# Kernel tuning notes

Hardware: AMD Instinct MI355X
Metric: run time of the kernel (lower is better)

Reference implementation:

```python
import jax, jax.numpy as jnp
import numpy as np

D_MODEL = 2048
D_LATENT = 512


def setup_inputs() -> dict:
    key = jax.random.key(0)
    ks = jax.random.split(key, 6)
    x = jax.random.normal(ks[0], (2, 4096, D_MODEL), dtype=jnp.float32)
    cache = jax.random.normal(ks[1], (2, 4096, D_LATENT), dtype=jnp.float32)
    s = 0.02
    # weights stored (in_features, out_features); equivalent to torch Linear (no bias)
    W_kv = jax.random.normal(ks[2], (D_MODEL, D_LATENT), dtype=jnp.float32) * s
    W_q = jax.random.normal(ks[3], (D_MODEL, D_MODEL), dtype=jnp.float32) * s
    W_lq = jax.random.normal(ks[4], (D_MODEL, D_LATENT), dtype=jnp.float32) * s
    W_o = jax.random.normal(ks[5], (D_LATENT, D_MODEL), dtype=jnp.float32) * s
    return {"x": x, "cache": cache, "W_kv": W_kv, "W_q": W_q, "W_lq": W_lq, "W_o": W_o}


def reference(x, cache, W_kv, W_q, W_lq, W_o):
    # latent compression of inputs: (B, S, d_latent)
    l_kv_new = jnp.einsum('bsd,dl->bsl', x, W_kv)
    # query path: x -> query (d_model) -> latent query (d_latent)
    q = jnp.einsum('bsd,de->bse', x, W_q)
    lq = jnp.einsum('bse,el->bsl', q, W_lq)
    # append to cache: (B, T+S, d_latent)
    l_kv = jnp.concatenate([cache, l_kv_new], axis=1)
    scale = jnp.sqrt(jnp.float32(D_LATENT)).astype(x.dtype)
    # attention in latent space: scores (B, S, T+S)
    scores = jnp.einsum('bsl,btl->bst', lq, l_kv) / scale
    weights = jax.nn.softmax(scores, axis=-1)
    ctx = jnp.einsum('bst,btl->bsl', weights, l_kv)
    out = jnp.einsum('bsl,ld->bsd', ctx, W_o)
    return out, l_kv
```

## Files before the change

kernel.cpp:

```cpp
#include <hip/hip_runtime.h>
#include <hip/hip_bf16.h>
#include <math.h>


typedef _Float16 f16x8 __attribute__((ext_vector_type(8)));
typedef _Float16 f16x4 __attribute__((ext_vector_type(4)));
typedef float    f32x4 __attribute__((ext_vector_type(4)));
typedef float    f32x8 __attribute__((ext_vector_type(8)));

__device__ __forceinline__ void gl_lds16(const void* g, void* l) {
  __builtin_amdgcn_global_load_lds(
      (const __attribute__((address_space(1))) void*)g,
      (__attribute__((address_space(3))) void*)l, 16, 0, 0);
}

__global__ __launch_bounds__(256) void k_cache(const float* __restrict__ cache,
                                               float* __restrict__ lkv_f32,
                                               _Float16* __restrict__ lkv16, int n4) {
  int i = blockIdx.x * blockDim.x + threadIdx.x;
  int st = gridDim.x * blockDim.x;
  for (; i < n4; i += st) {
    f32x4 v = reinterpret_cast<const f32x4*>(cache)[i];
    int e = i << 2;
    int b = e >> 21;
    int dst = e + (b << 21);
    *reinterpret_cast<f32x4*>(lkv_f32 + dst) = v;
    *reinterpret_cast<f16x4*>(lkv16 + dst) = __builtin_convertvector(v, f16x4);
  }
}

__global__ __launch_bounds__(256) void k_tc(const float* __restrict__ in,
                                            _Float16* __restrict__ out, int R, int C) {
  __shared__ float t[32][33];
  const int c0 = blockIdx.x << 5, r0 = blockIdx.y << 5;
  const int tid = threadIdx.x;
  {
    int r = tid >> 3, c4 = (tid & 7) << 2;
    f32x4 v = *reinterpret_cast<const f32x4*>(&in[(long)(r0 + r) * C + c0 + c4]);
    t[r][c4] = v[0]; t[r][c4 + 1] = v[1]; t[r][c4 + 2] = v[2]; t[r][c4 + 3] = v[3];
  }
  __syncthreads();
  {
    int c = tid >> 3, r4 = (tid & 7) << 2;
    f16x4 o = {(_Float16)t[r4][c], (_Float16)t[r4 + 1][c],
               (_Float16)t[r4 + 2][c], (_Float16)t[r4 + 3][c]};
    *reinterpret_cast<f16x4*>(&out[(long)(c0 + c) * R + r0 + r4]) = o;
  }
}

__global__ __launch_bounds__(256) void k_tb(const _Float16* __restrict__ in,
                                            _Float16* __restrict__ out, int R, int C) {
  __shared__ _Float16 t[32][36];
  const int c0 = blockIdx.x << 5, r0 = blockIdx.y << 5;
  const int tid = threadIdx.x;
  {
    int r = tid >> 3, c4 = (tid & 7) << 2;
    f16x4 v = *reinterpret_cast<const f16x4*>(&in[(long)(r0 + r) * C + c0 + c4]);
    t[r][c4] = v[0]; t[r][c4 + 1] = v[1]; t[r][c4 + 2] = v[2]; t[r][c4 + 3] = v[3];
  }
  __syncthreads();
  {
    int c = tid >> 3, r4 = (tid & 7) << 2;
    f16x4 o = {t[r4][c], t[r4 + 1][c], t[r4 + 2][c], t[r4 + 3][c]};
    *reinterpret_cast<f16x4*>(&out[(long)(c0 + c) * R + r0 + r4]) = o;
  }
}

template <int CMODE, int AF32, int BF32>
__global__ __launch_bounds__(256) void k_gemm(const void* __restrict__ Av,
                                              const void* __restrict__ Bv,
                                              float* __restrict__ Cf,
                                              _Float16* __restrict__ Ch,
                                              _Float16* __restrict__ Ch2,
                                              int M, int N, int K, int lda, int ldb,
                                              float cscale) {
  const _Float16* A16 = (const _Float16*)Av;
  const float*    A32 = (const float*)Av;
  const _Float16* B16 = (const _Float16*)Bv;
  const float*    B32 = (const float*)Bv;
  if constexpr (CMODE == 4 || CMODE == 7) {
    const long z = blockIdx.z;
    A16 += z * K; A32 += z * K;
    B16 += z * K; B32 += z * K;
    if constexpr (CMODE == 4) Cf += z * (long)M * N;
    else                      Ch += z * (long)M * N;
  }
  __shared__ alignas(16) _Float16 As[128 * 64];
  __shared__ alignas(16) _Float16 Bs[128 * 64];
  const int tid = threadIdx.x;
  const int lane = tid & 63;
  const int w = tid >> 6;
  const int wr = ((w >> 1) & 1) << 6, wc = (w & 1) << 6;
  const int bm = blockIdx.x << 7, bn = blockIdx.y << 7;
  const int g = lane >> 4, ln15 = lane & 15;

  f32x4 acc[4][4] = {};

  const int srowl = lane >> 3;
  const int skcol = (lane & 7) << 3;
  const int wofs = (srowl << 6) + (((lane & 7) ^ srowl) << 3);

  f16x8 ra[4], rb[4];
  auto loadregs = [&](int k0) {
#pragma unroll
    for (int i = 0; i < 4; ++i) {
      int ch = (w << 2) + i;
      int row = (ch << 3) + srowl;
      if constexpr (AF32) {
        f32x8 v = *reinterpret_cast<const f32x8*>(&A32[(long)(bm + row) * lda + k0 + skcol]);
        ra[i] = __builtin_convertvector(v, f16x8);
      } else {
        ra[i] = *reinterpret_cast<const f16x8*>(&A16[(long)(bm + row) * lda + k0 + skcol]);
      }
      if constexpr (BF32) {
        f32x8 v = *reinterpret_cast<const f32x8*>(&B32[(long)(bn + row) * ldb + k0 + skcol]);
        rb[i] = __builtin_convertvector(v, f16x8);
      } else {
        rb[i] = *reinterpret_cast<const f16x8*>(&B16[(long)(bn + row) * ldb + k0 + skcol]);
      }
    }
  };
  loadregs(0);
  const int nk = K >> 6;
  for (int kt = 0; kt < nk; ++kt) {
    __syncthreads();
#pragma unroll
    for (int i = 0; i < 4; ++i) {
      int ch = (w << 2) + i;
      *reinterpret_cast<f16x8*>(&As[(ch << 9) + wofs]) = ra[i];
      *reinterpret_cast<f16x8*>(&Bs[(ch << 9) + wofs]) = rb[i];
    }
    __syncthreads();
    if (kt + 1 < nk) loadregs((kt + 1) << 6);
#pragma unroll
    for (int ks = 0; ks < 2; ++ks) {
      f16x8 af[4], bf[4];
#pragma unroll
      for (int i = 0; i < 4; ++i) {
        const int arow = wr + (i << 4) + ln15;
        const int brow = wc + (i << 4) + ln15;
        const int inner = (((ks << 5) + (g << 3)) ^ ((ln15 & 7) << 3));
        af[i] = *reinterpret_cast<const f16x8*>(&As[arow * 64 + inner]);
        bf[i] = *reinterpret_cast<const f16x8*>(&Bs[brow * 64 + inner]);
      }
#pragma unroll
      for (int i = 0; i < 4; ++i)
#pragma unroll
        for (int j = 0; j < 4; ++j)
          acc[i][j] = __builtin_amdgcn_mfma_f32_16x16x32_f16(af[i], bf[j], acc[i][j], 0, 0, 0);
    }
  }
#pragma unroll
  for (int i = 0; i < 4; ++i) {
    const int row = bm + wr + (i << 4) + (g << 2);
#pragma unroll
    for (int j = 0; j < 4; ++j) {
      const int col = bn + wc + (j << 4) + ln15;
#pragma unroll
      for (int r = 0; r < 4; ++r) {
        float v = acc[i][j][r];
        long orow = row + r;
        if constexpr (CMODE == 2) {
          long m2 = ((orow >> 12) << 13) + 4096 + (orow & 4095);
          Cf[m2 * 512 + col] = v;
          Ch[m2 * 512 + col] = (_Float16)v;
        } else if constexpr (CMODE == 1) {
          Ch[orow * N + col] = (_Float16)v;
        } else if constexpr (CMODE == 3) {
          Ch[orow * N + col] = (_Float16)(v * cscale);
        } else if constexpr (CMODE == 5) {
          if (col < 512) {
            Ch[orow * 512 + col] = (_Float16)v;
          } else {
            long m2 = ((orow >> 12) << 13) + 4096 + (orow & 4095);
            Cf[m2 * 512 + (col - 512)] = v;
            Ch2[m2 * 512 + (col - 512)] = (_Float16)v;
          }
        } else if constexpr (CMODE == 7) {
          Ch[orow * N + col] = (_Float16)v;
        } else {
          Cf[orow * N + col] = v;
        }
      }
    }
  }
}

template <int CMODE, int STATS>
__global__ __launch_bounds__(512, 2) void k_gemm256(const _Float16* __restrict__ A,
                                                    const _Float16* __restrict__ B,
                                                    float* __restrict__ Cf,
                                                    _Float16* __restrict__ Ch,
                                                    float* __restrict__ Lp,
                                                    int M, int N, int K,
                                                    int lda, int ldb) {
  extern __shared__ _Float16 sm[];
  _Float16* As = sm;
  _Float16* Bs = sm + 32768;
  const int tid = threadIdx.x;
  const int lane = tid & 63;
  const int w = tid >> 6;
  const int wm = w >> 2, wn = w & 3;
  const int bm = blockIdx.x << 8, bn = blockIdx.y << 8;
  const int g = lane >> 4, ln15 = lane & 15;

  f32x4 acc[8][4] = {};

  const int lrow8 = lane >> 3;
  const int lswz  = ((lane & 7) ^ lrow8) << 3;
  const _Float16* Ap[4];
  const _Float16* Bp[4];
  int loff[4];
#pragma unroll
  for (int i = 0; i < 4; ++i) {
    const int row = (i << 6) + (w << 3) + lrow8;
    Ap[i] = &A[(long)(bm + row) * lda + lswz];
    Bp[i] = &B[(long)(bn + row) * ldb + lswz];
    loff[i] = ((i << 6) + (w << 3)) << 6;
  }

  auto stage = [&](int buf, int kt) {
    const int k0 = kt << 6;
    const int bo = buf << 14;
#pragma unroll
    for (int i = 0; i < 4; ++i) {
      gl_lds16(Ap[i] + k0, &As[bo + loff[i]]);
      gl_lds16(Bp[i] + k0, &Bs[bo + loff[i]]);
    }
  };

  const int nk = K >> 6;
  stage(0, 0);
  if (nk > 1) stage(1, 1);

  for (int kt = 0; kt < nk; ++kt) {
    if (kt + 1 < nk) asm volatile("s_waitcnt vmcnt(8)" ::: "memory");
    else             asm volatile("s_waitcnt vmcnt(0)" ::: "memory");
    __builtin_amdgcn_sched_barrier(0);
    __builtin_amdgcn_s_barrier();
    const int bo = (kt & 1) << 14;
#pragma unroll
    for (int ks = 0; ks < 2; ++ks) {
      f16x8 af[8], bf[4];
      const int innersw = ((ks << 5) + (g << 3)) ^ ((ln15 & 7) << 3);
#pragma unroll
      for (int i = 0; i < 8; ++i) {
        const int arow = (wm << 7) + (i << 4) + ln15;
        af[i] = *reinterpret_cast<const f16x8*>(&As[bo + arow * 64 + innersw]);
      }
#pragma unroll
      for (int j = 0; j < 4; ++j) {
        const int brow = (wn << 6) + (j << 4) + ln15;
        bf[j] = *reinterpret_cast<const f16x8*>(&Bs[bo + brow * 64 + innersw]);
      }
#pragma unroll
      for (int i = 0; i < 8; ++i)
#pragma unroll
        for (int j = 0; j < 4; ++j)
          acc[i][j] = __builtin_amdgcn_mfma_f32_16x16x32_f16(af[i], bf[j], acc[i][j], 0, 0, 0);
    }
    asm volatile("s_waitcnt lgkmcnt(0)" ::: "memory");
    __builtin_amdgcn_sched_barrier(0);
    __builtin_amdgcn_s_barrier();
    if (kt + 2 < nk) stage(kt & 1, kt + 2);
  }

  if constexpr (STATS) {
    float* Lsh = (float*)sm;
    float part[8][4];
#pragma unroll
    for (int i = 0; i < 8; ++i) {
      const int row = bm + (wm << 7) + (i << 4) + (g << 2);
#pragma unroll
      for (int r = 0; r < 4; ++r) {
        float s = 0.f;
#pragma unroll
        for (int j = 0; j < 4; ++j) {
          const int col = bn + (wn << 6) + (j << 4) + ln15;
          float e = fminf(__expf(acc[i][j][r]), 60000.f);
          Ch[(long)(row + r) * N + col] = (_Float16)e;
          s += e;
        }
#pragma unroll
        for (int off = 1; off < 16; off <<= 1) s += __shfl_xor(s, off);
        part[i][r] = s;
      }
    }
    if (ln15 == 0) {
#pragma unroll
      for (int i = 0; i < 8; ++i)
#pragma unroll
        for (int r = 0; r < 4; ++r) {
          const int lrow = (wm << 7) + (i << 4) + (g << 2) + r;
          Lsh[(lrow << 2) + wn] = part[i][r];
        }
    }
    __syncthreads();
    if (tid < 256) {
      float L = Lsh[(tid << 2)] + Lsh[(tid << 2) + 1] +
                Lsh[(tid << 2) + 2] + Lsh[(tid << 2) + 3];
      Lp[(long)(bm + tid) * gridDim.y + blockIdx.y] = L;
    }
  } else {
#pragma unroll
    for (int i = 0; i < 8; ++i) {
      const int row = bm + (wm << 7) + (i << 4) + (g << 2);
#pragma unroll
      for (int j = 0; j < 4; ++j) {
        const int col = bn + (wn << 6) + (j << 4) + ln15;
#pragma unroll
        for (int r = 0; r < 4; ++r) {
          if constexpr (CMODE == 1)
            Ch[(long)(row + r) * N + col] = (_Float16)acc[i][j][r];
          else
            Cf[(long)(row + r) * N + col] = acc[i][j][r];
        }
      }
    }
  }
}

__global__ __launch_bounds__(256) void k_linv(const float* __restrict__ Lp,
                                              float* __restrict__ Linv, int nb) {
  const int r = (blockIdx.x << 8) + threadIdx.x;
  float s = 0.f;
  for (int i = 0; i < nb; ++i) s += Lp[(long)r * nb + i];
  Linv[r] = 1.f / s;
}

__global__ __launch_bounds__(256) void k_red4(const float* __restrict__ p,
                                              _Float16* __restrict__ o,
                                              int n4, float scale) {
  const f32x4* pv = reinterpret_cast<const f32x4*>(p);
  int i = blockIdx.x * blockDim.x + threadIdx.x;
  int st = gridDim.x * blockDim.x;
  for (; i < n4; i += st) {
    f32x4 a = pv[i] + pv[i + n4] + pv[i + 2 * n4] + pv[i + 3 * n4];
    a *= scale;
    reinterpret_cast<f16x4*>(o)[i] = __builtin_convertvector(a, f16x4);
  }
}

__global__ __launch_bounds__(256) void k_red4row(const _Float16* __restrict__ p,
                                                 const float* __restrict__ Linv,
                                                 _Float16* __restrict__ o, int n4) {
  const f16x4* pv = reinterpret_cast<const f16x4*>(p);
  int i = blockIdx.x * blockDim.x + threadIdx.x;
  int st = gridDim.x * blockDim.x;
  for (; i < n4; i += st) {
    f32x4 a = __builtin_convertvector(pv[i], f32x4) +
              __builtin_convertvector(pv[i + n4], f32x4) +
              __builtin_convertvector(pv[i + 2 * n4], f32x4) +
              __builtin_convertvector(pv[i + 3 * n4], f32x4);
    a *= Linv[i >> 7];
    reinterpret_cast<f16x4*>(o)[i] = __builtin_convertvector(a, f16x4);
  }
}


extern "C" void kernel_launch(void* const* d_in, const int* in_sizes, int n_in,
                              void* d_out, int out_size, void* d_ws, size_t ws_size,
                              hipStream_t stream) {
  const float* x     = (const float*)d_in[0];
  const float* cache = (const float*)d_in[1];
  const float* W_kv  = (const float*)d_in[2];
  const float* W_q   = (const float*)d_in[3];
  const float* W_lq  = (const float*)d_in[4];
  const float* W_o   = (const float*)d_in[5];

  float* out     = (float*)d_out;
  float* lkv_out = out + (size_t)8192 * 2048;

  _Float16* base16 = (_Float16*)d_out;
  _Float16* lq16   = base16 + 16777216;
  _Float16* WlqT   = base16 + 25165824;
  _Float16* WcombT = base16 + 26214400;
  _Float16* WkvT   = base16 + 27262976;
  _Float16* lkvT16 = base16 + 20971520;
  _Float16* PVp16  = base16;
  float*    Lp     = (float*)(base16 + 29360128);
  float*    Linv   = Lp + 131072;

  _Float16* lkv16 = (_Float16*)d_ws;
  _Float16* ctx   = lkv16 + 8388608;
  _Float16* WoT   = ctx + 4194304;
  _Float16* Sbuf  = WoT + 1048576;
  float*    Wcp   = (float*)Sbuf;

  const size_t sbase = 27262976;
  int CR = 1024;
  if (ws_size >= sbase + (size_t)4096 * 8192 * 2) CR = 4096;
  else if (ws_size >= sbase + (size_t)2048 * 8192 * 2) CR = 2048;

  const float iscale = 0.044194173824159216f;

  hipFuncSetAttribute((const void*)k_gemm256<1, 1>,
                      hipFuncAttributeMaxDynamicSharedMemorySize, 131072);
  hipFuncSetAttribute((const void*)k_gemm256<0, 0>,
                      hipFuncAttributeMaxDynamicSharedMemorySize, 131072);

  k_cache<<<1024, 256, 0, stream>>>(cache, lkv_out, lkv16, 4194304 / 4);
  k_tc<<<dim3(16, 64), 256, 0, stream>>>(W_kv, WkvT, 2048, 512);
  k_tc<<<dim3(16, 64), 256, 0, stream>>>(W_lq, WlqT, 2048, 512);
  k_tc<<<dim3(64, 16), 256, 0, stream>>>(W_o, WoT, 512, 2048);

  k_gemm<4, 0, 1><<<dim3(4, 16, 4), 256, 0, stream>>>(
      WlqT, W_q, Wcp, nullptr, nullptr, 512, 2048, 512, 2048, 2048, 1.f);
  k_red4<<<1024, 256, 0, stream>>>(Wcp, WcombT, (512 * 2048) / 4, iscale);
  k_gemm<5, 1, 0><<<dim3(64, 8), 256, 0, stream>>>(
      x, WcombT, lkv_out, lq16, lkv16, 8192, 1024, 2048, 2048, 2048, 1.f);
  k_tb<<<dim3(16, 512), 256, 0, stream>>>(lkv16, lkvT16, 16384, 512);

  for (long r0 = 0; r0 < 8192; r0 += CR) {
    const long b = r0 >> 12;
    k_gemm256<1, 1><<<dim3(CR >> 8, 32), 512, 131072, stream>>>(
        lq16 + r0 * 512, lkv16 + b * 8192 * 512, nullptr, Sbuf, Lp,
        CR, 8192, 512, 512, 512);
    k_linv<<<CR >> 8, 256, 0, stream>>>(Lp, Linv, 32);
    k_gemm<7, 0, 0><<<dim3(CR >> 7, 4, 4), 256, 0, stream>>>(
        Sbuf, lkvT16 + b * 8192, nullptr, PVp16, nullptr,
        CR, 512, 2048, 8192, 16384, 1.f);
    k_red4row<<<2048, 256, 0, stream>>>(PVp16, Linv, ctx + r0 * 512, (CR * 512) / 4);
  }

  k_gemm256<0, 0><<<dim3(32, 8), 512, 131072, stream>>>(ctx, WoT, out, nullptr,
                                                        nullptr,
                                                        8192, 2048, 512, 512, 512);
}
```

Baseline: 336.2 us.

## Pre-convert x to fp16 and add XCD-aware block swizzle to GEMMs

Adds a separate kernel that converts x from fp32 to fp16 into scratch space in the output buffer. The fused projection GEMM then reads fp16 A operands instead of converting fp32 tiles in its load path. Workgroup indices are also remapped so that consecutive tiles land on the same XCD, which targets better L2 locality on MI355X for the 128-tile projection GEMM and all 256-tile GEMMs. The trade is an extra 64MB read plus 32MB write pass over x in exchange for cheaper operand loads.

```diff
diff --git a/kernel.cpp b/kernel.cpp
--- a/kernel.cpp
+++ b/kernel.cpp
@@ -12,6 +12,17 @@
   __builtin_amdgcn_global_load_lds(
       (const __attribute__((address_space(1))) void*)g,
       (__attribute__((address_space(3))) void*)l, 16, 0, 0);
+}
+
+
+__global__ __launch_bounds__(256) void k_cvt(const float* __restrict__ in,
+                                             _Float16* __restrict__ out, int n4) {
+  int i = blockIdx.x * blockDim.x + threadIdx.x;
+  int st = gridDim.x * blockDim.x;
+  for (; i < n4; i += st) {
+    f32x4 v = reinterpret_cast<const f32x4*>(in)[i];
+    reinterpret_cast<f16x4*>(out)[i] = __builtin_convertvector(v, f16x4);
+  }
 }
 
 __global__ __launch_bounds__(256) void k_cache(const float* __restrict__ cache,
@@ -66,7 +77,7 @@
   }
 }
 
-template <int CMODE, int AF32, int BF32>
+template <int CMODE, int AF32, int BF32, int SWZ>
 __global__ __launch_bounds__(256) void k_gemm(const void* __restrict__ Av,
                                               const void* __restrict__ Bv,
                                               float* __restrict__ Cf,
@@ -85,13 +96,23 @@
     if constexpr (CMODE == 4) Cf += z * (long)M * N;
     else                      Ch += z * (long)M * N;
   }
+  int bxr = blockIdx.x, byr = blockIdx.y;
+  if constexpr (SWZ) {
+    const int nbx = gridDim.x, nby = gridDim.y, nwg = nbx * nby;
+    if ((nwg & 7) == 0) {
+      const int orig = bxr * nby + byr;
+      const int q = nwg >> 3;
+      const int wg = (orig & 7) * q + (orig >> 3);
+      bxr = wg / nby; byr = wg % nby;
+    }
+  }
   __shared__ alignas(16) _Float16 As[128 * 64];
   __shared__ alignas(16) _Float16 Bs[128 * 64];
   const int tid = threadIdx.x;
   const int lane = tid & 63;
   const int w = tid >> 6;
   const int wr = ((w >> 1) & 1) << 6, wc = (w & 1) << 6;
-  const int bm = blockIdx.x << 7, bn = blockIdx.y << 7;
+  const int bm = bxr << 7, bn = byr << 7;
   const int g = lane >> 4, ln15 = lane & 15;
 
   f32x4 acc[4][4] = {};
@@ -197,11 +218,21 @@
   extern __shared__ _Float16 sm[];
   _Float16* As = sm;
   _Float16* Bs = sm + 32768;
+  int bxr = blockIdx.x, byr = blockIdx.y;
+  {
+    const int nbx = gridDim.x, nby = gridDim.y, nwg = nbx * nby;
+    if ((nwg & 7) == 0) {
+      const int orig = bxr * nby + byr;
+      const int q = nwg >> 3;
+      const int wg = (orig & 7) * q + (orig >> 3);
+      bxr = wg / nby; byr = wg % nby;
+    }
+  }
   const int tid = threadIdx.x;
   const int lane = tid & 63;
   const int w = tid >> 6;
   const int wm = w >> 2, wn = w & 3;
-  const int bm = blockIdx.x << 8, bn = blockIdx.y << 8;
+  const int bm = bxr << 8, bn = byr << 8;
   const int g = lane >> 4, ln15 = lane & 15;
 
   f32x4 acc[8][4] = {};
@@ -299,7 +330,7 @@
     if (tid < 256) {
       float L = Lsh[(tid << 2)] + Lsh[(tid << 2) + 1] +
                 Lsh[(tid << 2) + 2] + Lsh[(tid << 2) + 3];
-      Lp[(long)(bm + tid) * gridDim.y + blockIdx.y] = L;
+      Lp[(long)(bm + tid) * gridDim.y + byr] = L;
     }
   } else {
 #pragma unroll
@@ -372,6 +403,7 @@
   float* lkv_out = out + (size_t)8192 * 2048;
 
   _Float16* base16 = (_Float16*)d_out;
+  _Float16* x16    = base16;
   _Float16* lq16   = base16 + 16777216;
   _Float16* WlqT   = base16 + 25165824;
   _Float16* WcombT = base16 + 26214400;
@@ -399,16 +431,17 @@
   hipFuncSetAttribute((const void*)k_gemm256<0, 0>,
                       hipFuncAttributeMaxDynamicSharedMemorySize, 131072);
 
+  k_cvt<<<1024, 256, 0, stream>>>(x, x16, 16777216 / 4);
   k_cache<<<1024, 256, 0, stream>>>(cache, lkv_out, lkv16, 4194304 / 4);
   k_tc<<<dim3(16, 64), 256, 0, stream>>>(W_kv, WkvT, 2048, 512);
   k_tc<<<dim3(16, 64), 256, 0, stream>>>(W_lq, WlqT, 2048, 512);
   k_tc<<<dim3(64, 16), 256, 0, stream>>>(W_o, WoT, 512, 2048);
 
-  k_gemm<4, 0, 1><<<dim3(4, 16, 4), 256, 0, stream>>>(
+  k_gemm<4, 0, 1, 0><<<dim3(4, 16, 4), 256, 0, stream>>>(
       WlqT, W_q, Wcp, nullptr, nullptr, 512, 2048, 512, 2048, 2048, 1.f);
   k_red4<<<1024, 256, 0, stream>>>(Wcp, WcombT, (512 * 2048) / 4, iscale);
-  k_gemm<5, 1, 0><<<dim3(64, 8), 256, 0, stream>>>(
-      x, WcombT, lkv_out, lq16, lkv16, 8192, 1024, 2048, 2048, 2048, 1.f);
+  k_gemm<5, 0, 0, 1><<<dim3(64, 8), 256, 0, stream>>>(
+      x16, WcombT, lkv_out, lq16, lkv16, 8192, 1024, 2048, 2048, 2048, 1.f);
   k_tb<<<dim3(16, 512), 256, 0, stream>>>(lkv16, lkvT16, 16384, 512);
 
   for (long r0 = 0; r0 < 8192; r0 += CR) {
@@ -417,7 +450,7 @@
         lq16 + r0 * 512, lkv16 + b * 8192 * 512, nullptr, Sbuf, Lp,
         CR, 8192, 512, 512, 512);
     k_linv<<<CR >> 8, 256, 0, stream>>>(Lp, Linv, 32);
-    k_gemm<7, 0, 0><<<dim3(CR >> 7, 4, 4), 256, 0, stream>>>(
+    k_gemm<7, 0, 0, 0><<<dim3(CR >> 7, 4, 4), 256, 0, stream>>>(
         Sbuf, lkvT16 + b * 8192, nullptr, PVp16, nullptr,
         CR, 512, 2048, 8192, 16384, 1.f);
     k_red4row<<<2048, 256, 0, stream>>>(PVp16, Linv, ctx + r0 * 512, (CR * 512) / 4);
```

New measurement: 336.2 us. About the same (+0.0%).
